# Performance work log

Hardware: AMD Instinct MI355X
Metric: run time of the kernel (lower is better)

The kernel has to match this reference:

```python
import jax, jax.numpy as jnp
import numpy as np

B, N = 2048, 8192


def setup_inputs() -> dict:
    key = jax.random.key(0)
    k1, k2 = jax.random.split(key)
    output = jax.random.uniform(k1, (B, N, 1), dtype=jnp.float32)
    labels = jax.random.randint(k2, (B, N), 0, 2, dtype=jnp.int32)
    return {"output": output, "labels": labels}


def _f1_grid(labels):
    # labels: [B, N] binary relevance. Returns F1@cut(j+1) for every j. [B, N]
    lab = labels.astype(jnp.float32)
    cum = jnp.cumsum(lab, axis=1)                      # rel found in top j+1
    k = jnp.arange(1, lab.shape[1] + 1, dtype=jnp.float32)  # cut depth j+1
    total = jnp.sum(lab, axis=1, keepdims=True)        # total relevant per list
    prec = cum / k
    rec = jnp.where(total > 0, cum / jnp.maximum(total, 1.0), 0.0)
    denom = prec + rec
    return jnp.where(denom > 0, 2.0 * prec * rec / jnp.maximum(denom, 1e-30), 0.0)


def reference(output, labels) -> jnp.ndarray:
    # r[i][j] = f1(labels[i], j); loss = -sum(output * r) / B
    r = _f1_grid(labels)                               # [B, N]
    out = jnp.squeeze(output, axis=2)                  # [B, N]
    return -jnp.sum(out * r) / out.shape[0]
```

## Files before the change

### kernel.cpp

```cpp
#include <hip/hip_runtime.h>


#define BLOCK 256
#define NROW 8192
#define PASSES 8

__device__ __forceinline__ int mbcnt64(unsigned long long m) {
    return __builtin_amdgcn_mbcnt_hi((unsigned)(m >> 32),
           __builtin_amdgcn_mbcnt_lo((unsigned)m, 0u));
}

__global__ __launch_bounds__(BLOCK) void f1_row_kernel(
    const float* __restrict__ outv,
    const int* __restrict__ labels,
    float* __restrict__ partials)
{
    const int row  = blockIdx.x;
    const int t    = threadIdx.x;
    const int lane = t & 63;
    const int wid  = t >> 6;

    const long long rowbase = (long long)row * NROW;
    const int4*   lab4 = (const int4*)(labels + rowbase);
    const float4* op4  = (const float4*)(outv + rowbase);

    __shared__ int wave_tot[PASSES][4];

    int4   lv[PASSES];
    float4 ov[PASSES];
    #pragma unroll
    for (int p = 0; p < PASSES; ++p) lv[p] = lab4[p * 256 + t];
    #pragma unroll
    for (int p = 0; p < PASSES; ++p) ov[p] = op4[p * 256 + t];

    unsigned int mask = 0;
    int pre[PASSES];
    #pragma unroll
    for (int p = 0; p < PASSES; ++p) {
        const int b0 = (lv[p].x != 0), b1 = (lv[p].y != 0),
                  b2 = (lv[p].z != 0), b3 = (lv[p].w != 0);
        mask |= (unsigned)(b0 | (b1 << 1) | (b2 << 2) | (b3 << 3)) << (p * 4);
        const unsigned long long m0 = __ballot(b0);
        const unsigned long long m1 = __ballot(b1);
        const unsigned long long m2 = __ballot(b2);
        const unsigned long long m3 = __ballot(b3);
        pre[p] = mbcnt64(m0) + mbcnt64(m1) + mbcnt64(m2) + mbcnt64(m3);
        if (lane == 0) {
            wave_tot[p][wid] = __popcll(m0) + __popcll(m1) + __popcll(m2) + __popcll(m3);
        }
    }
    __syncthreads();

    int base[PASSES];
    int run = 0;
    #pragma unroll
    for (int p = 0; p < PASSES; ++p) {
        const int w0 = wave_tot[p][0], w1 = wave_tot[p][1],
                  w2 = wave_tot[p][2], w3 = wave_tot[p][3];
        const int wb = (wid > 0 ? w0 : 0) + (wid > 1 ? w1 : 0) + (wid > 2 ? w2 : 0);
        base[p] = run + wb + pre[p];
        run += w0 + w1 + w2 + w3;
    }
    const float ftot = (float)run;

    float acc = 0.f;
    #pragma unroll
    for (int p = 0; p < PASSES; ++p) {
        int c = base[p];
        const int kbase = p * 1024 + t * 4;
        const unsigned nib = (mask >> (p * 4)) & 0xFu;
        c += (nib & 1u);
        acc = fmaf(ov[p].x, (float)(2 * c) * __builtin_amdgcn_rcpf((float)(kbase + 1) + ftot), acc);
        c += (nib >> 1) & 1u;
        acc = fmaf(ov[p].y, (float)(2 * c) * __builtin_amdgcn_rcpf((float)(kbase + 2) + ftot), acc);
        c += (nib >> 2) & 1u;
        acc = fmaf(ov[p].z, (float)(2 * c) * __builtin_amdgcn_rcpf((float)(kbase + 3) + ftot), acc);
        c += (nib >> 3) & 1u;
        acc = fmaf(ov[p].w, (float)(2 * c) * __builtin_amdgcn_rcpf((float)(kbase + 4) + ftot), acc);
    }

    #pragma unroll
    for (int off = 32; off > 0; off >>= 1) acc += __shfl_down(acc, off, 64);
    __shared__ float wacc[4];
    if (lane == 0) wacc[wid] = acc;
    __syncthreads();
    if (t == 0) partials[row] = wacc[0] + wacc[1] + wacc[2] + wacc[3];
}

__global__ __launch_bounds__(256) void f1_finalize_kernel(
    const float* __restrict__ partials, float* __restrict__ out, int B)
{
    double s = 0.0;
    for (int i = threadIdx.x; i < B; i += 256) s += (double)partials[i];
    #pragma unroll
    for (int off = 32; off > 0; off >>= 1) s += __shfl_down(s, off, 64);
    __shared__ double ws[4];
    const int lane = threadIdx.x & 63, wid = threadIdx.x >> 6;
    if (lane == 0) ws[wid] = s;
    __syncthreads();
    if (threadIdx.x == 0) {
        out[0] = (float)(-(ws[0] + ws[1] + ws[2] + ws[3]) / (double)B);
    }
}

extern "C" void kernel_launch(void* const* d_in, const int* in_sizes, int n_in,
                              void* d_out, int out_size, void* d_ws, size_t ws_size,
                              hipStream_t stream) {
    const float* outv   = (const float*)d_in[0];
    const int*   labels = (const int*)d_in[1];
    float* partials = (float*)d_ws;
    float* result   = (float*)d_out;

    const int B = 2048;
    f1_row_kernel<<<B, BLOCK, 0, stream>>>(outv, labels, partials);
    f1_finalize_kernel<<<1, 256, 0, stream>>>(partials, result, B);
}
```

Baseline: 146.4 us.

## Assign one row per wavefront with double-buffered streaming loads

Each wavefront now processes a full row of 8192 elements, so the per-block LDS exchange and __syncthreads barriers go away. There are 4 rows per block and a quarter as many blocks. Labels are streamed in groups of 8 int4 per lane with double buffering, and the relevance bits are packed into two 64-bit masks. The F1 pass then streams the output values the same way, recomputing prefix counts with ballot and mbcnt. The goal is to remove block-level synchronization and overlap loads with compute, at the cost of fewer blocks, longer serial work per wave, and repeated ballots.

```diff
diff --git a/kernel.cpp b/kernel.cpp
--- a/kernel.cpp
+++ b/kernel.cpp
@@ -1,9 +1,12 @@
 #include <hip/hip_runtime.h>
 
 
-#define BLOCK 256
 #define NROW 8192
-#define PASSES 8
+#define WAVES_PER_BLOCK 4
+#define BLOCK (64 * WAVES_PER_BLOCK)
+#define NCHUNK 32
+#define GRP 8
+#define NGRP (NCHUNK / GRP)
 
 __device__ __forceinline__ int mbcnt64(unsigned long long m) {
     return __builtin_amdgcn_mbcnt_hi((unsigned)(m >> 32),
@@ -15,76 +18,102 @@
     const int* __restrict__ labels,
     float* __restrict__ partials)
 {
-    const int row  = blockIdx.x;
     const int t    = threadIdx.x;
     const int lane = t & 63;
     const int wid  = t >> 6;
+    const int row  = blockIdx.x * WAVES_PER_BLOCK + wid;
 
     const long long rowbase = (long long)row * NROW;
     const int4*   lab4 = (const int4*)(labels + rowbase);
     const float4* op4  = (const float4*)(outv + rowbase);
 
-    __shared__ int wave_tot[PASSES][4];
+    unsigned long long mlo = 0ull, mhi = 0ull;
+    int run = 0;
 
-    int4   lv[PASSES];
-    float4 ov[PASSES];
+    int4 bufA[GRP], bufB[GRP];
     #pragma unroll
-    for (int p = 0; p < PASSES; ++p) lv[p] = lab4[p * 256 + t];
+    for (int i = 0; i < GRP; ++i) bufA[i] = lab4[i * 64 + lane];
+
     #pragma unroll
-    for (int p = 0; p < PASSES; ++p) ov[p] = op4[p * 256 + t];
-
-    unsigned int mask = 0;
-    int pre[PASSES];
-    #pragma unroll
-    for (int p = 0; p < PASSES; ++p) {
-        const int b0 = (lv[p].x != 0), b1 = (lv[p].y != 0),
-                  b2 = (lv[p].z != 0), b3 = (lv[p].w != 0);
-        mask |= (unsigned)(b0 | (b1 << 1) | (b2 << 2) | (b3 << 3)) << (p * 4);
-        const unsigned long long m0 = __ballot(b0);
-        const unsigned long long m1 = __ballot(b1);
-        const unsigned long long m2 = __ballot(b2);
-        const unsigned long long m3 = __ballot(b3);
-        pre[p] = mbcnt64(m0) + mbcnt64(m1) + mbcnt64(m2) + mbcnt64(m3);
-        if (lane == 0) {
-            wave_tot[p][wid] = __popcll(m0) + __popcll(m1) + __popcll(m2) + __popcll(m3);
+    for (int g = 0; g < NGRP - 1; ++g) {
+        #pragma unroll
+        for (int i = 0; i < GRP; ++i) {
+            const int4 v = lab4[(g + 1) * GRP * 64 + i * 64 + lane];
+            if (g & 1) bufA[i] = v; else bufB[i] = v;
+        }
+        #pragma unroll
+        for (int i = 0; i < GRP; ++i) {
+            const int4 lv = (g & 1) ? bufB[i] : bufA[i];
+            const int c = g * GRP + i;
+            const int b0 = (lv.x != 0), b1 = (lv.y != 0), b2 = (lv.z != 0), b3 = (lv.w != 0);
+            const unsigned long long m0 = __ballot(b0), m1 = __ballot(b1),
+                                     m2 = __ballot(b2), m3 = __ballot(b3);
+            run += __popcll(m0) + __popcll(m1) + __popcll(m2) + __popcll(m3);
+            const unsigned long long nib =
+                (unsigned long long)(b0 | (b1 << 1) | (b2 << 2) | (b3 << 3));
+            if (c < 16) mlo |= nib << (c * 4); else mhi |= nib << ((c - 16) * 4);
         }
     }
-    __syncthreads();
 
-    int base[PASSES];
-    int run = 0;
+    float4 fA[GRP], fB[GRP];
     #pragma unroll
-    for (int p = 0; p < PASSES; ++p) {
-        const int w0 = wave_tot[p][0], w1 = wave_tot[p][1],
-                  w2 = wave_tot[p][2], w3 = wave_tot[p][3];
-        const int wb = (wid > 0 ? w0 : 0) + (wid > 1 ? w1 : 0) + (wid > 2 ? w2 : 0);
-        base[p] = run + wb + pre[p];
-        run += w0 + w1 + w2 + w3;
+    for (int i = 0; i < GRP; ++i) fA[i] = op4[i * 64 + lane];
+
+    {
+        const int g = NGRP - 1;
+        #pragma unroll
+        for (int i = 0; i < GRP; ++i) {
+            const int4 lv = (g & 1) ? bufB[i] : bufA[i];
+            const int c = g * GRP + i;
+            const int b0 = (lv.x != 0), b1 = (lv.y != 0), b2 = (lv.z != 0), b3 = (lv.w != 0);
+            const unsigned long long m0 = __ballot(b0), m1 = __ballot(b1),
+                                     m2 = __ballot(b2), m3 = __ballot(b3);
+            run += __popcll(m0) + __popcll(m1) + __popcll(m2) + __popcll(m3);
+            const unsigned long long nib =
+                (unsigned long long)(b0 | (b1 << 1) | (b2 << 2) | (b3 << 3));
+            if (c < 16) mlo |= nib << (c * 4); else mhi |= nib << ((c - 16) * 4);
+        }
     }
+
     const float ftot = (float)run;
 
     float acc = 0.f;
+    int runbase = 0;
     #pragma unroll
-    for (int p = 0; p < PASSES; ++p) {
-        int c = base[p];
-        const int kbase = p * 1024 + t * 4;
-        const unsigned nib = (mask >> (p * 4)) & 0xFu;
-        c += (nib & 1u);
-        acc = fmaf(ov[p].x, (float)(2 * c) * __builtin_amdgcn_rcpf((float)(kbase + 1) + ftot), acc);
-        c += (nib >> 1) & 1u;
-        acc = fmaf(ov[p].y, (float)(2 * c) * __builtin_amdgcn_rcpf((float)(kbase + 2) + ftot), acc);
-        c += (nib >> 2) & 1u;
-        acc = fmaf(ov[p].z, (float)(2 * c) * __builtin_amdgcn_rcpf((float)(kbase + 3) + ftot), acc);
-        c += (nib >> 3) & 1u;
-        acc = fmaf(ov[p].w, (float)(2 * c) * __builtin_amdgcn_rcpf((float)(kbase + 4) + ftot), acc);
+    for (int g = 0; g < NGRP; ++g) {
+        if (g + 1 < NGRP) {
+            #pragma unroll
+            for (int i = 0; i < GRP; ++i) {
+                const float4 v = op4[(g + 1) * GRP * 64 + i * 64 + lane];
+                if (g & 1) fA[i] = v; else fB[i] = v;
+            }
+        }
+        #pragma unroll
+        for (int i = 0; i < GRP; ++i) {
+            const float4 ov = (g & 1) ? fB[i] : fA[i];
+            const int c = g * GRP + i;
+            const unsigned nib = (unsigned)(((c < 16) ? (mlo >> (c * 4))
+                                                      : (mhi >> ((c - 16) * 4))) & 0xFull);
+            const int b0 = nib & 1, b1 = (nib >> 1) & 1, b2 = (nib >> 2) & 1, b3 = (nib >> 3) & 1;
+            const unsigned long long m0 = __ballot(b0), m1 = __ballot(b1),
+                                     m2 = __ballot(b2), m3 = __ballot(b3);
+            int cum = runbase + mbcnt64(m0) + mbcnt64(m1) + mbcnt64(m2) + mbcnt64(m3);
+            const int kbase = c * 256 + lane * 4;
+            cum += b0;
+            acc = fmaf(ov.x, (float)(2 * cum) * __builtin_amdgcn_rcpf((float)(kbase + 1) + ftot), acc);
+            cum += b1;
+            acc = fmaf(ov.y, (float)(2 * cum) * __builtin_amdgcn_rcpf((float)(kbase + 2) + ftot), acc);
+            cum += b2;
+            acc = fmaf(ov.z, (float)(2 * cum) * __builtin_amdgcn_rcpf((float)(kbase + 3) + ftot), acc);
+            cum += b3;
+            acc = fmaf(ov.w, (float)(2 * cum) * __builtin_amdgcn_rcpf((float)(kbase + 4) + ftot), acc);
+            runbase += __popcll(m0) + __popcll(m1) + __popcll(m2) + __popcll(m3);
+        }
     }
 
     #pragma unroll
     for (int off = 32; off > 0; off >>= 1) acc += __shfl_down(acc, off, 64);
-    __shared__ float wacc[4];
-    if (lane == 0) wacc[wid] = acc;
-    __syncthreads();
-    if (t == 0) partials[row] = wacc[0] + wacc[1] + wacc[2] + wacc[3];
+    if (lane == 0) partials[row] = acc;
 }
 
 __global__ __launch_bounds__(256) void f1_finalize_kernel(
@@ -112,6 +141,6 @@
     float* result   = (float*)d_out;
 
     const int B = 2048;
-    f1_row_kernel<<<B, BLOCK, 0, stream>>>(outv, labels, partials);
+    f1_row_kernel<<<B / WAVES_PER_BLOCK, BLOCK, 0, stream>>>(outv, labels, partials);
     f1_finalize_kernel<<<1, 256, 0, stream>>>(partials, result, B);
 }
```

Measured after the change: 144.6 us. No clear change (-1.2%).
